# Kernel optimization log

Hardware: AMD Instinct MI355X
Metric: run time of the kernel (lower is better)

## Reference

```python
import jax, jax.numpy as jnp
import numpy as np

B, V = 256, 128000


def setup_inputs() -> dict:
    key = jax.random.key(0)
    k1, k2 = jax.random.split(key)
    logits = jax.random.normal(k1, (B, V), dtype=jnp.float32) * 4.0
    # temperatures in [0.3, 1.2] to avoid division by ~0
    temperatures = jax.random.uniform(k2, (B,), dtype=jnp.float32) * 0.9 + 0.3
    return {"logits": logits, "temperatures": temperatures}


def reference(logits, temperatures):
    # temperature-scaled softmax
    x = logits.astype(jnp.float32) / temperatures[:, None]
    probs = jax.nn.softmax(x, axis=-1)  # (B, V)
    # torch.empty_like(probs).exponential_(1).clamp_min_(1e-10)
    noise = jnp.maximum(
        jax.random.exponential(jax.random.key(42), probs.shape, dtype=jnp.float32),
        1e-10,
    )
    # Gumbel-max style sampling: argmax of probs / Exp(1) noise
    return jnp.argmax(probs / noise, axis=-1)  # (B,) int
```

## Files before the change

kernel.cpp:

```cpp
#include <hip/hip_runtime.h>
#include <stdint.h>
#include <math.h>

#define BB 256
#define VV 128000
#define THREADS 1024
#define WAVES (THREADS / 64)

__device__ __forceinline__ void threefry_0_42(uint32_t x0, uint32_t x1,
                                              uint32_t& o0, uint32_t& o1) {
    const uint32_t k0 = 0u;
    const uint32_t k1 = 42u;
    const uint32_t k2 = 0x1BD11BDAu ^ k0 ^ k1;

    x0 += k0;
    x1 += k1;

#define TF_ROUND(r)                                  \
    do {                                             \
        x0 += x1;                                    \
        x1 = (x1 << (r)) | (x1 >> (32 - (r)));       \
        x1 ^= x0;                                    \
    } while (0)

    TF_ROUND(13); TF_ROUND(15); TF_ROUND(26); TF_ROUND(6);
    x0 += k1; x1 += k2 + 1u;
    TF_ROUND(17); TF_ROUND(29); TF_ROUND(16); TF_ROUND(24);
    x0 += k2; x1 += k0 + 2u;
    TF_ROUND(13); TF_ROUND(15); TF_ROUND(26); TF_ROUND(6);
    x0 += k0; x1 += k1 + 3u;
    TF_ROUND(17); TF_ROUND(29); TF_ROUND(16); TF_ROUND(24);
    x0 += k1; x1 += k2 + 4u;
    TF_ROUND(13); TF_ROUND(15); TF_ROUND(26); TF_ROUND(6);
    x0 += k2; x1 += k0 + 5u;
#undef TF_ROUND

    o0 = x0;
    o1 = x1;
}

__device__ __forceinline__ uint32_t f2o(float f) {
    uint32_t u = __float_as_uint(f);
    return (u & 0x80000000u) ? ~u : (u | 0x80000000u);
}

__device__ __forceinline__ float log_exp_noise(uint32_t bits) {
    const float uf = __uint_as_float(0x3F800000u | (bits >> 9));
    const float u = uf - 1.0f;
    const float m = 2.0f - uf;
    const float lg_m = __builtin_amdgcn_logf(m);
    const float es =
        u * fmaf(u, fmaf(u, fmaf(u, fmaf(u, 0.2f, 0.25f), 0.33333333333f), 0.5f), 1.0f);
    const bool small = (u < 0.0625f);
    float P = small ? es : -lg_m;
    const float csel = small ? 0.0f : -0.36651292058166432701f;
    P = fmaxf(P, 1e-10f);
    return fmaf(0.69314718055994530942f, __builtin_amdgcn_logf(P), csel);
}

__global__ __launch_bounds__(THREADS, 4) void sampler_kernel(
    const float* __restrict__ logits,
    const float* __restrict__ temps,
    int* __restrict__ out) {
    const int b = blockIdx.x;
    const float invT = 1.0f / temps[b];
    const float* row = logits + (size_t)b * VV;
    const uint32_t ibase = (uint32_t)b * (uint32_t)VV;

    float best_s = -INFINITY;
    uint32_t best_v = 0u;

    const int tid = threadIdx.x;

#pragma unroll 1
    for (int base = 0; base < VV; base += THREADS * 8) {
        const int i1 = base + tid * 4;
        const int i2 = base + THREADS * 4 + tid * 4;

        if (i1 < VV) {
            const float4 x4 = *reinterpret_cast<const float4*>(row + i1);
            const float xs[4] = {x4.x, x4.y, x4.z, x4.w};
#pragma unroll
            for (int j = 0; j < 4; ++j) {
                const uint32_t v = (uint32_t)i1 + (uint32_t)j;
                uint32_t o0, o1;
                threefry_0_42(0u, ibase + v, o0, o1);
                const float lnE = log_exp_noise(o0 ^ o1);
                const float s = fmaf(xs[j], invT, -lnE);
                if (s > best_s) { best_s = s; best_v = v; }
            }
        }
        if (i2 < VV) {
            const float4 x4 = *reinterpret_cast<const float4*>(row + i2);
            const float xs[4] = {x4.x, x4.y, x4.z, x4.w};
#pragma unroll
            for (int j = 0; j < 4; ++j) {
                const uint32_t v = (uint32_t)i2 + (uint32_t)j;
                uint32_t o0, o1;
                threefry_0_42(0u, ibase + v, o0, o1);
                const float lnE = log_exp_noise(o0 ^ o1);
                const float s = fmaf(xs[j], invT, -lnE);
                if (s > best_s) { best_s = s; best_v = v; }
            }
        }
    }

    unsigned long long best =
        ((unsigned long long)f2o(best_s) << 32) | (uint32_t)(~best_v);

#pragma unroll
    for (int off = 32; off >= 1; off >>= 1) {
        const unsigned long long o = __shfl_xor(best, off);
        best = (o > best) ? o : best;
    }

    __shared__ unsigned long long sbest[WAVES];
    const int lane = tid & 63;
    const int wid = tid >> 6;
    if (lane == 0) sbest[wid] = best;
    __syncthreads();

    if (tid == 0) {
        unsigned long long r = sbest[0];
#pragma unroll
        for (int w = 1; w < WAVES; ++w) r = (sbest[w] > r) ? sbest[w] : r;
        out[b] = (int)(~(uint32_t)(r & 0xFFFFFFFFull));
    }
}

extern "C" void kernel_launch(void* const* d_in, const int* in_sizes, int n_in,
                              void* d_out, int out_size, void* d_ws, size_t ws_size,
                              hipStream_t stream) {
    const float* logits = (const float*)d_in[0];
    const float* temps = (const float*)d_in[1];
    int* out = (int*)d_out;

    hipLaunchKernelGGL(sampler_kernel, dim3(BB), dim3(THREADS), 0, stream,
                       logits, temps, out);
}
```

Baseline: 95.65 us.

## Split each row across four blocks and combine partial argmax in second kernel

Each row is now processed by four 512-thread blocks instead of one 1024-thread block, giving 1024 blocks so the grid fills the GPU's CUs more evenly. Each block writes a packed score/index partial to workspace, and a small second kernel reduces the four partials per row. The threefry hash is also restructured to process four counters in lockstep with constant-folded keys, exposing more instruction-level parallelism. The cost is an extra kernel launch and a workspace round trip.

```diff
diff --git a/kernel.cpp b/kernel.cpp
--- a/kernel.cpp
+++ b/kernel.cpp
@@ -3,40 +3,61 @@
 #include <math.h>
 
 #define BB 256
-#define VV 128000
-#define THREADS 1024
+#define ROW 128000
+#define SPLIT 4
+#define CHUNK (ROW / SPLIT)
+#define THREADS 512
 #define WAVES (THREADS / 64)
+#define GRID (BB * SPLIT)
 
-__device__ __forceinline__ void threefry_0_42(uint32_t x0, uint32_t x1,
-                                              uint32_t& o0, uint32_t& o1) {
-    const uint32_t k0 = 0u;
-    const uint32_t k1 = 42u;
-    const uint32_t k2 = 0x1BD11BDAu ^ k0 ^ k1;
+__device__ __forceinline__ uint32_t rotl32(uint32_t x, int r) {
+    return (x << r) | (x >> (32 - r));
+}
 
-    x0 += k0;
-    x1 += k1;
+#define TF_K2 0x1BD11BF0u
 
-#define TF_ROUND(r)                                  \
-    do {                                             \
-        x0 += x1;                                    \
-        x1 = (x1 << (r)) | (x1 >> (32 - (r)));       \
-        x1 ^= x0;                                    \
+__device__ __forceinline__ void threefry4_xor(uint32_t c, uint32_t bits[4]) {
+    uint32_t x0[4], x1[4];
+#pragma unroll
+    for (int j = 0; j < 4; ++j) {
+        x0[j] = 0u;
+        x1[j] = c + (uint32_t)j + 42u;
+    }
+
+#define ROUND4(r)                                     \
+    do {                                              \
+        _Pragma("unroll")                             \
+        for (int j = 0; j < 4; ++j) {                 \
+            x0[j] += x1[j];                           \
+            x1[j] = rotl32(x1[j], (r));               \
+            x1[j] ^= x0[j];                           \
+        }                                             \
+    } while (0)
+#define INJ4(a, b)                                    \
+    do {                                              \
+        _Pragma("unroll")                             \
+        for (int j = 0; j < 4; ++j) {                 \
+            x0[j] += (a);                             \
+            x1[j] += (b);                             \
+        }                                             \
     } while (0)
 
-    TF_ROUND(13); TF_ROUND(15); TF_ROUND(26); TF_ROUND(6);
-    x0 += k1; x1 += k2 + 1u;
-    TF_ROUND(17); TF_ROUND(29); TF_ROUND(16); TF_ROUND(24);
-    x0 += k2; x1 += k0 + 2u;
-    TF_ROUND(13); TF_ROUND(15); TF_ROUND(26); TF_ROUND(6);
-    x0 += k0; x1 += k1 + 3u;
-    TF_ROUND(17); TF_ROUND(29); TF_ROUND(16); TF_ROUND(24);
-    x0 += k1; x1 += k2 + 4u;
-    TF_ROUND(13); TF_ROUND(15); TF_ROUND(26); TF_ROUND(6);
-    x0 += k2; x1 += k0 + 5u;
-#undef TF_ROUND
+    ROUND4(13); ROUND4(15); ROUND4(26); ROUND4(6);
+    INJ4(42u, TF_K2 + 1u);
+    ROUND4(17); ROUND4(29); ROUND4(16); ROUND4(24);
+    INJ4(TF_K2, 2u);
+    ROUND4(13); ROUND4(15); ROUND4(26); ROUND4(6);
+    INJ4(0u, 45u);
+    ROUND4(17); ROUND4(29); ROUND4(16); ROUND4(24);
+    INJ4(42u, TF_K2 + 4u);
+    ROUND4(13); ROUND4(15); ROUND4(26); ROUND4(6);
+    INJ4(TF_K2, 5u);
 
-    o0 = x0;
-    o1 = x1;
+#undef ROUND4
+#undef INJ4
+
+#pragma unroll
+    for (int j = 0; j < 4; ++j) bits[j] = x0[j] ^ x1[j];
 }
 
 __device__ __forceinline__ uint32_t f2o(float f) {
@@ -58,49 +79,40 @@
     return fmaf(0.69314718055994530942f, __builtin_amdgcn_logf(P), csel);
 }
 
-__global__ __launch_bounds__(THREADS, 4) void sampler_kernel(
+__global__ __launch_bounds__(THREADS, 8) void sampler_kernel(
     const float* __restrict__ logits,
     const float* __restrict__ temps,
-    int* __restrict__ out) {
-    const int b = blockIdx.x;
+    unsigned long long* __restrict__ ws) {
+    const int g = blockIdx.x;
+    const int b = g >> 2;
+    const int q = g & 3;
     const float invT = 1.0f / temps[b];
-    const float* row = logits + (size_t)b * VV;
-    const uint32_t ibase = (uint32_t)b * (uint32_t)VV;
+    const float* rowp = logits + (size_t)b * ROW + (size_t)q * CHUNK;
+    const uint32_t cbase = (uint32_t)b * (uint32_t)ROW + (uint32_t)q * CHUNK;
 
     float best_s = -INFINITY;
     uint32_t best_v = 0u;
-
     const int tid = threadIdx.x;
 
 #pragma unroll 1
-    for (int base = 0; base < VV; base += THREADS * 8) {
-        const int i1 = base + tid * 4;
-        const int i2 = base + THREADS * 4 + tid * 4;
+    for (int t = 0; t < (CHUNK + THREADS * 4 - 1) / (THREADS * 4); ++t) {
+        const int vl = t * THREADS * 4 + tid * 4;
+        if (vl < CHUNK) {
+            const float4 x4 = *reinterpret_cast<const float4*>(rowp + vl);
+            const float xs[4] = {x4.x, x4.y, x4.z, x4.w};
 
-        if (i1 < VV) {
-            const float4 x4 = *reinterpret_cast<const float4*>(row + i1);
-            const float xs[4] = {x4.x, x4.y, x4.z, x4.w};
+            uint32_t bits[4];
+            threefry4_xor(cbase + (uint32_t)vl, bits);
+
+            float s[4];
+#pragma unroll
+            for (int j = 0; j < 4; ++j)
+                s[j] = fmaf(xs[j], invT, -log_exp_noise(bits[j]));
+
 #pragma unroll
             for (int j = 0; j < 4; ++j) {
-                const uint32_t v = (uint32_t)i1 + (uint32_t)j;
-                uint32_t o0, o1;
-                threefry_0_42(0u, ibase + v, o0, o1);
-                const float lnE = log_exp_noise(o0 ^ o1);
-                const float s = fmaf(xs[j], invT, -lnE);
-                if (s > best_s) { best_s = s; best_v = v; }
-            }
-        }
-        if (i2 < VV) {
-            const float4 x4 = *reinterpret_cast<const float4*>(row + i2);
-            const float xs[4] = {x4.x, x4.y, x4.z, x4.w};
-#pragma unroll
-            for (int j = 0; j < 4; ++j) {
-                const uint32_t v = (uint32_t)i2 + (uint32_t)j;
-                uint32_t o0, o1;
-                threefry_0_42(0u, ibase + v, o0, o1);
-                const float lnE = log_exp_noise(o0 ^ o1);
-                const float s = fmaf(xs[j], invT, -lnE);
-                if (s > best_s) { best_s = s; best_v = v; }
+                const uint32_t v = (uint32_t)(q * CHUNK + vl) + (uint32_t)j;
+                if (s[j] > best_s) { best_s = s[j]; best_v = v; }
             }
         }
     }
@@ -124,8 +136,18 @@
         unsigned long long r = sbest[0];
 #pragma unroll
         for (int w = 1; w < WAVES; ++w) r = (sbest[w] > r) ? sbest[w] : r;
-        out[b] = (int)(~(uint32_t)(r & 0xFFFFFFFFull));
+        ws[g] = r;
     }
+}
+
+__global__ __launch_bounds__(BB) void combine_kernel(
+    const unsigned long long* __restrict__ ws, int* __restrict__ out) {
+    const int b = threadIdx.x;
+    const unsigned long long* p = ws + b * SPLIT;
+    unsigned long long r = p[0];
+#pragma unroll
+    for (int w = 1; w < SPLIT; ++w) r = (p[w] > r) ? p[w] : r;
+    out[b] = (int)(~(uint32_t)(r & 0xFFFFFFFFull));
 }
 
 extern "C" void kernel_launch(void* const* d_in, const int* in_sizes, int n_in,
@@ -134,7 +156,9 @@
     const float* logits = (const float*)d_in[0];
     const float* temps = (const float*)d_in[1];
     int* out = (int*)d_out;
+    unsigned long long* ws = (unsigned long long*)d_ws;
 
-    hipLaunchKernelGGL(sampler_kernel, dim3(BB), dim3(THREADS), 0, stream,
-                       logits, temps, out);
+    hipLaunchKernelGGL(sampler_kernel, dim3(GRID), dim3(THREADS), 0, stream,
+                       logits, temps, ws);
+    hipLaunchKernelGGL(combine_kernel, dim3(1), dim3(BB), 0, stream, ws, out);
 }
```

After: 93.52 us. 2.2% less time.
